# Kernel tuning notes

Measured on AMD Instinct MI355X. Metric: run time of the kernel, lower is better.

## Reference

```python
import jax, jax.numpy as jnp
import numpy as np

EMB = 1024
HEAD = 64


def setup_inputs() -> dict:
    key = jax.random.key(0)
    kx, kq, kk, kv = jax.random.split(key, 4)
    x = jax.random.normal(kx, (4, 4096, EMB), dtype=jnp.float32)
    # nn.Linear(emb, head, bias=False): y = x @ W^T; store transposed [emb, head]
    s = 1.0 / np.sqrt(EMB)
    Wq = jax.random.uniform(kq, (EMB, HEAD), jnp.float32, -s, s)
    Wk = jax.random.uniform(kk, (EMB, HEAD), jnp.float32, -s, s)
    Wv = jax.random.uniform(kv, (EMB, HEAD), jnp.float32, -s, s)
    return {"x": x, "Wq": Wq, "Wk": Wk, "Wv": Wv}


def reference(x, Wq, Wk, Wv):
    # x: [B, T, E]; projections -> [B, T, H]
    Q = jnp.einsum("bte,eh->bth", x, Wq)
    K = jnp.einsum("bte,eh->bth", x, Wk)
    V = jnp.einsum("bte,eh->bth", x, Wv)
    scale = 1.0 / np.sqrt(HEAD).astype(np.float32)
    scores = jnp.einsum("bqh,bkh->bqk", Q, K) * scale  # [B, T, T]
    attn = jax.nn.softmax(scores, axis=-1)
    out = jnp.einsum("bqk,bkh->bqh", attn, V)  # [B, T, H]
    return out
```

## Files before the change

kernel.cpp:

```cpp
#include <hip/hip_runtime.h>
#include <hip/hip_bf16.h>

typedef __bf16 bf16x8 __attribute__((ext_vector_type(8)));
typedef float floatx4 __attribute__((ext_vector_type(4)));

#define B_ 4
#define T_ 4096
#define E_ 1024
#define H_ 64
#define NSEG 8
#define SEGLEN (T_ / NSEG)
#define NROWS (B_ * T_)

#define QSCALE 0.18033688011112042f

#if __has_builtin(__builtin_amdgcn_exp2f)
#define EXP2(x) __builtin_amdgcn_exp2f(x)
#else
#define EXP2(x) exp2f(x)
#endif

__device__ __forceinline__ floatx4 mfma16(bf16x8 a, bf16x8 b, floatx4 c) {
  return __builtin_amdgcn_mfma_f32_16x16x32_bf16(a, b, c, 0, 0, 0);
}

#define GLDS16(gp, lp)                                                        \
  __builtin_amdgcn_global_load_lds(                                           \
      (const __attribute__((address_space(1))) void*)(gp),                    \
      (__attribute__((address_space(3))) void*)(lp), 16, 0, 0)

#define WAITCNT_VM(n) asm volatile("s_waitcnt vmcnt(" #n ")" ::: "memory")
#define WAITCNT_LGKM0 asm volatile("s_waitcnt lgkmcnt(0)" ::: "memory")

__global__ void prep_wt_k(const float* __restrict__ Wq, const float* __restrict__ Wk,
                          const float* __restrict__ Wv, __bf16* __restrict__ Wfrag) {
  int gid = blockIdx.x * 4 + (threadIdx.x >> 6);
  int lane = threadIdx.x & 63;
  int ch = gid / 24, rem = gid % 24;
  int nt = rem >> 1, half = rem & 1;
  int g = lane >> 4, lm = lane & 15;
  int w = nt >> 2;
  const float* W = (w == 0) ? Wq : (w == 1) ? Wk : Wv;
  float sc = (w == 0) ? QSCALE : 1.0f;
  int h = (nt & 3) * 16 + lm;
  int e0 = ch * 64 + half * 32 + g * 8;
  __bf16* dst = Wfrag + (size_t)gid * 1024 / 2 + lane * 8;
  bf16x8 v;
#pragma unroll
  for (int j = 0; j < 8; j++) v[j] = (__bf16)(W[(size_t)(e0 + j) * H_ + h] * sc);
  *(bf16x8*)dst = v;
}

__global__ __launch_bounds__(256) void proj_k(
    const float* __restrict__ x, const __bf16* __restrict__ Wfrag,
    __bf16* __restrict__ Qo, __bf16* __restrict__ Ko, __bf16* __restrict__ Vt) {
  __shared__ __align__(16) char sW[2 * 24576];
  __shared__ __align__(16) char sX[2 * 4096];

  int tid = threadIdx.x;
  int wv = tid >> 6, lane = tid & 63;
  int lm = lane & 15, g = lane >> 4;
  int row_base = blockIdx.x * 32;

  const char* wfb = (const char*)Wfrag;

  int xrow = tid >> 3, xc = tid & 7;
  const float* xsrc = x + (size_t)(row_base + xrow) * E_ + xc * 8;
  int xw_off = xrow * 128 + ((xc ^ (xrow & 7)) << 4);

  int aoff[2][2];
#pragma unroll
  for (int rg = 0; rg < 2; rg++)
#pragma unroll
    for (int ks = 0; ks < 2; ks++)
      aoff[rg][ks] = (rg * 16 + lm) * 128 + ((((ks << 2) + g) ^ (lm & 7)) << 4);

#define STAGE_W(buf, ch)                                                      \
  _Pragma("unroll") for (int j = 0; j < 6; j++)                               \
      GLDS16(wfb + (size_t)(ch) * 24576 + j * 4096 + tid * 16,                \
             sW + (buf) * 24576 + j * 4096 + tid * 16);

#define CVT_X(fA, fB, xv)                                                     \
  {                                                                           \
    xv[0] = (__bf16)fA.x; xv[1] = (__bf16)fA.y;                               \
    xv[2] = (__bf16)fA.z; xv[3] = (__bf16)fA.w;                               \
    xv[4] = (__bf16)fB.x; xv[5] = (__bf16)fB.y;                               \
    xv[6] = (__bf16)fB.z; xv[7] = (__bf16)fB.w;                               \
  }

  floatx4 acc[2][3];
#pragma unroll
  for (int rg = 0; rg < 2; rg++)
#pragma unroll
    for (int i = 0; i < 3; i++) acc[rg][i] = (floatx4)0.0f;

  float4 fA = *(const float4*)(xsrc);
  float4 fB = *(const float4*)(xsrc + 4);
  STAGE_W(0, 0);
  WAITCNT_VM(6);
  __builtin_amdgcn_sched_barrier(0);
  {
    bf16x8 xv; CVT_X(fA, fB, xv);
    *(bf16x8*)(sX + xw_off) = xv;
  }
  WAITCNT_LGKM0;

  for (int ch = 0; ch < 16; ch++) {
    if (ch < 15) {
      fA = *(const float4*)(xsrc + (ch + 1) * 64);
      fB = *(const float4*)(xsrc + (ch + 1) * 64 + 4);
      STAGE_W((ch + 1) & 1, ch + 1);
      WAITCNT_VM(8);
    } else {
      WAITCNT_VM(0);
    }
    __builtin_amdgcn_sched_barrier(0);
    __builtin_amdgcn_s_barrier();

    const char* wB = sW + (ch & 1) * 24576 + (size_t)(wv * 3 * 2) * 1024 + lane * 16;
    const char* xB = sX + (ch & 1) * 4096;
    bf16x8 a[2][2];
#pragma unroll
    for (int rg = 0; rg < 2; rg++)
#pragma unroll
      for (int ks = 0; ks < 2; ks++)
        a[rg][ks] = *(const bf16x8*)(xB + aoff[rg][ks]);
#pragma unroll
    for (int i = 0; i < 3; i++) {
      bf16x8 b0 = *(const bf16x8*)(wB + (size_t)(i * 2) * 1024);
      bf16x8 b1 = *(const bf16x8*)(wB + (size_t)(i * 2 + 1) * 1024);
#pragma unroll
      for (int rg = 0; rg < 2; rg++) {
        acc[rg][i] = mfma16(a[rg][0], b0, acc[rg][i]);
        acc[rg][i] = mfma16(a[rg][1], b1, acc[rg][i]);
      }
    }

    if (ch < 15) {
      WAITCNT_VM(6);
      __builtin_amdgcn_sched_barrier(0);
      bf16x8 xv; CVT_X(fA, fB, xv);
      *(bf16x8*)(sX + ((ch + 1) & 1) * 4096 + xw_off) = xv;
      WAITCNT_LGKM0;
      __builtin_amdgcn_s_barrier();
    }
  }

#pragma unroll
  for (int i = 0; i < 3; i++) {
    int nt = wv * 3 + i;
    int w = nt >> 2;
    int h = (nt & 3) * 16 + lm;
#pragma unroll
    for (int rg = 0; rg < 2; rg++)
#pragma unroll
      for (int r = 0; r < 4; r++) {
        __bf16 v = (__bf16)acc[rg][i][r];
        int rr = row_base + rg * 16 + g * 4 + r;
        if (w == 0)      Qo[(size_t)rr * H_ + h] = v;
        else if (w == 1) Ko[(size_t)rr * H_ + h] = v;
        else {
          int b = rr >> 12, t = rr & (T_ - 1);
          int kin = t & 63;
          int pos = ((kin >> 5) << 5) + (((kin >> 2) & 3) << 3) +
                    (((kin >> 4) & 1) << 2) + (kin & 3);
          Vt[((size_t)b * H_ + h) * T_ + (t & ~63) + pos] = v;
        }
      }
  }
}

__global__ __launch_bounds__(256, 2) void attn_k(
    const __bf16* __restrict__ Q, const __bf16* __restrict__ K,
    const __bf16* __restrict__ Vt, __bf16* __restrict__ Op, float* __restrict__ lp) {
  __shared__ __align__(16) char sK[2 * 8192];
  __shared__ __align__(16) char sV[2 * 8192];

  int qb = blockIdx.x, b = blockIdx.y, seg = blockIdx.z;
  int tid = threadIdx.x, wv = tid >> 6, lane = tid & 63;
  int lm = lane & 15, g = lane >> 4;
  int q0 = qb * 256 + wv * 64;

  const __bf16* Qb = Q + (size_t)b * T_ * H_;
  const char* Kb = (const char*)(K + (size_t)b * T_ * H_);
  const char* Vb = (const char*)(Vt + (size_t)b * H_ * T_);

  bf16x8 qf[4][2];
#pragma unroll
  for (int qi = 0; qi < 4; qi++)
#pragma unroll
    for (int hs = 0; hs < 2; hs++)
      qf[qi][hs] =
          *(const bf16x8*)&Qb[(size_t)(q0 + qi * 16 + lm) * H_ + hs * 32 + g * 8];

  floatx4 o_acc[4][4], o_l[4];
#pragma unroll
  for (int qi = 0; qi < 4; qi++) {
#pragma unroll
    for (int i = 0; i < 4; i++) o_acc[qi][i] = (floatx4)0.0f;
    o_l[qi] = (floatx4)0.0f;
  }

  bf16x8 vone;
#pragma unroll
  for (int j = 0; j < 8; j++) vone[j] = (__bf16)1.0f;

  int s3 = lm & 7;
  int koff[4][2], voff[2][4];
#pragma unroll
  for (int mt = 0; mt < 4; mt++) {
    koff[mt][0] = (mt * 16 + lm) * 128 + ((g ^ s3) << 4);
    koff[mt][1] = (mt * 16 + lm) * 128 + (((g + 4) ^ s3) << 4);
  }
#pragma unroll
  for (int ks = 0; ks < 2; ks++)
#pragma unroll
    for (int nt = 0; nt < 4; nt++)
      voff[ks][nt] = (nt * 16 + lm) * 128 + (((ks * 4 + g) ^ s3) << 4);

  int srow = tid >> 3, schk = tid & 7;
  int swz0 = (schk ^ (srow & 7)) << 4;

#define ATTN_STAGE(buf, k0_)                                                  \
  {                                                                           \
    int off = (buf) * 8192 + tid * 16;                                        \
    GLDS16(Kb + (size_t)(k0_ + srow) * 128 + swz0, sK + off);                 \
    GLDS16(Kb + (size_t)(k0_ + srow + 32) * 128 + swz0, sK + off + 4096);     \
    GLDS16(Vb + (size_t)srow * (T_ * 2) + (size_t)(k0_) * 2 + swz0, sV + off);\
    GLDS16(Vb + (size_t)(srow + 32) * (T_ * 2) + (size_t)(k0_) * 2 + swz0,    \
           sV + off + 4096);                                                  \
  }

  int kbase = seg * SEGLEN;
  ATTN_STAGE(0, kbase);
  __syncthreads();

  for (int t = 0; t < SEGLEN / 64; t++) {
    if (t + 1 < SEGLEN / 64) ATTN_STAGE((t + 1) & 1, kbase + (t + 1) * 64);
    const char* kB = sK + (t & 1) * 8192;
    const char* vB = sV + (t & 1) * 8192;

    floatx4 s_acc[4][4];
#pragma unroll
    for (int mt = 0; mt < 4; mt++)
#pragma unroll
      for (int qi = 0; qi < 4; qi++) s_acc[mt][qi] = (floatx4)0.0f;
#pragma unroll
    for (int mt = 0; mt < 4; mt++) {
      bf16x8 a0 = *(const bf16x8*)(kB + koff[mt][0]);
      bf16x8 a1 = *(const bf16x8*)(kB + koff[mt][1]);
#pragma unroll
      for (int qi = 0; qi < 4; qi++) {
        s_acc[mt][qi] = mfma16(a0, qf[qi][0], s_acc[mt][qi]);
        s_acc[mt][qi] = mfma16(a1, qf[qi][1], s_acc[mt][qi]);
      }
    }

    bf16x8 pa[4][2];
#pragma unroll
    for (int qi = 0; qi < 4; qi++)
#pragma unroll
      for (int mt = 0; mt < 4; mt++)
#pragma unroll
        for (int r = 0; r < 4; r++)
          pa[qi][mt >> 1][(mt & 1) * 4 + r] = (__bf16)EXP2(s_acc[mt][qi][r]);

#pragma unroll
    for (int ks = 0; ks < 2; ks++) {
      bf16x8 bb[4];
#pragma unroll
      for (int nt = 0; nt < 4; nt++) bb[nt] = *(const bf16x8*)(vB + voff[ks][nt]);
#pragma unroll
      for (int qi = 0; qi < 4; qi++) {
#pragma unroll
        for (int nt = 0; nt < 4; nt++)
          o_acc[qi][nt] = mfma16(pa[qi][ks], bb[nt], o_acc[qi][nt]);
        o_l[qi] = mfma16(pa[qi][ks], vone, o_l[qi]);
      }
    }
    __syncthreads();
  }

  size_t rowbase = (size_t)seg * NROWS + (size_t)b * T_ + qb * 256 + wv * 64;
#pragma unroll
  for (int qi = 0; qi < 4; qi++) {
#pragma unroll
    for (int nt = 0; nt < 4; nt++)
#pragma unroll
      for (int r = 0; r < 4; r++)
        Op[(rowbase + qi * 16 + g * 4 + r) * 64 + nt * 16 + lm] =
            (__bf16)o_acc[qi][nt][r];
    if (lm == 0) {
#pragma unroll
      for (int r = 0; r < 4; r++)
        lp[rowbase + qi * 16 + g * 4 + r] = o_l[qi][r];
    }
  }
}

__global__ void combine_k(const __bf16* __restrict__ Op, const float* __restrict__ lp,
                          float* __restrict__ out) {
  int base = (blockIdx.x * 256 + threadIdx.x) * 8;
  int row = base >> 6;
  float L = 0.0f;
  float o[8];
#pragma unroll
  for (int j = 0; j < 8; j++) o[j] = 0.0f;
#pragma unroll
  for (int s = 0; s < NSEG; s++) {
    L += lp[(size_t)s * NROWS + row];
    bf16x8 v = *(const bf16x8*)&Op[(size_t)s * NROWS * 64 + base];
#pragma unroll
    for (int j = 0; j < 8; j++) o[j] += (float)v[j];
  }
  float inv = 1.0f / L;
  float4 r0 = {o[0] * inv, o[1] * inv, o[2] * inv, o[3] * inv};
  float4 r1 = {o[4] * inv, o[5] * inv, o[6] * inv, o[7] * inv};
  *(float4*)&out[base] = r0;
  *(float4*)&out[base + 4] = r1;
}

extern "C" void kernel_launch(void* const* d_in, const int* in_sizes, int n_in,
                              void* d_out, int out_size, void* d_ws, size_t ws_size,
                              hipStream_t stream) {
  const float* x  = (const float*)d_in[0];
  const float* Wq = (const float*)d_in[1];
  const float* Wk = (const float*)d_in[2];
  const float* Wv = (const float*)d_in[3];
  float* out = (float*)d_out;

  char* ws = (char*)d_ws;
  __bf16* Wf  = (__bf16*)(ws);
  __bf16* Qs  = (__bf16*)(ws + 0x60000);
  __bf16* Ks  = (__bf16*)(ws + 0x260000);
  __bf16* Vts = (__bf16*)(ws + 0x460000);
  __bf16* Op  = (__bf16*)(ws + 0x660000);
  float*  lp  = (float*)(ws + 0x1660000);

  prep_wt_k<<<96, 256, 0, stream>>>(Wq, Wk, Wv, Wf);
  proj_k<<<NROWS / 32, 256, 0, stream>>>(x, Wf, Qs, Ks, Vts);
  attn_k<<<dim3(T_ / 256, B_, NSEG), 256, 0, stream>>>(Qs, Ks, Vts, Op, lp);
  combine_k<<<NROWS * 64 / (256 * 8), 256, 0, stream>>>(Op, lp, out);
}
```

Before: 56.34 us.

## Stage fp32 x via direct-to-LDS loads and keep weight fragments in registers

```diff
diff --git a/kernel.cpp b/kernel.cpp
--- a/kernel.cpp
+++ b/kernel.cpp
@@ -30,7 +30,6 @@
       (__attribute__((address_space(3))) void*)(lp), 16, 0, 0)
 
 #define WAITCNT_VM(n) asm volatile("s_waitcnt vmcnt(" #n ")" ::: "memory")
-#define WAITCNT_LGKM0 asm volatile("s_waitcnt lgkmcnt(0)" ::: "memory")
 
 __global__ void prep_wt_k(const float* __restrict__ Wq, const float* __restrict__ Wk,
                           const float* __restrict__ Wv, __bf16* __restrict__ Wfrag) {
@@ -51,84 +50,82 @@
   *(bf16x8*)dst = v;
 }
 
-__global__ __launch_bounds__(256) void proj_k(
+__global__ __launch_bounds__(256, 2) void proj_k(
     const float* __restrict__ x, const __bf16* __restrict__ Wfrag,
     __bf16* __restrict__ Qo, __bf16* __restrict__ Ko, __bf16* __restrict__ Vt) {
-  __shared__ __align__(16) char sW[2 * 24576];
-  __shared__ __align__(16) char sX[2 * 4096];
+  __shared__ __align__(16) char sX[4 * 8192];
 
   int tid = threadIdx.x;
   int wv = tid >> 6, lane = tid & 63;
   int lm = lane & 15, g = lane >> 4;
   int row_base = blockIdx.x * 32;
 
-  const char* wfb = (const char*)Wfrag;
-
-  int xrow = tid >> 3, xc = tid & 7;
-  const float* xsrc = x + (size_t)(row_base + xrow) * E_ + xc * 8;
-  int xw_off = xrow * 128 + ((xc ^ (xrow & 7)) << 4);
-
-  int aoff[2][2];
+  const char* xb = (const char*)x;
+  const char* wfb = (const char*)Wfrag + (size_t)(wv * 3 * 2) * 1024 + lane * 16;
+
+  int xrow[2], xswz[2];
+#pragma unroll
+  for (int i = 0; i < 2; i++) {
+    int s = i * 256 + tid;
+    xrow[i] = s >> 4;
+    xswz[i] = ((s & 15) ^ (xrow[i] & 15)) << 4;
+  }
+
+#define STAGE_X(buf, ch)                                                      \
+  _Pragma("unroll") for (int i = 0; i < 2; i++)                               \
+      GLDS16(xb + (size_t)(row_base + xrow[i]) * 4096 + (size_t)(ch) * 256 +  \
+                 xswz[i],                                                     \
+             sX + (buf) * 8192 + (i * 256 + tid) * 16);
+
+  bf16x8 wreg[2][6];
+#define LOAD_W(set, ch)                                                       \
+  _Pragma("unroll") for (int j = 0; j < 6; j++)                               \
+      wreg[set][j] = *(const bf16x8*)(wfb + ((size_t)(ch) * 24 + j) * 1024);
+
+  floatx4 acc[2][3];
 #pragma unroll
   for (int rg = 0; rg < 2; rg++)
 #pragma unroll
-    for (int ks = 0; ks < 2; ks++)
-      aoff[rg][ks] = (rg * 16 + lm) * 128 + ((((ks << 2) + g) ^ (lm & 7)) << 4);
-
-#define STAGE_W(buf, ch)                                                      \
-  _Pragma("unroll") for (int j = 0; j < 6; j++)                               \
-      GLDS16(wfb + (size_t)(ch) * 24576 + j * 4096 + tid * 16,                \
-             sW + (buf) * 24576 + j * 4096 + tid * 16);
-
-#define CVT_X(fA, fB, xv)                                                     \
-  {                                                                           \
-    xv[0] = (__bf16)fA.x; xv[1] = (__bf16)fA.y;                               \
-    xv[2] = (__bf16)fA.z; xv[3] = (__bf16)fA.w;                               \
-    xv[4] = (__bf16)fB.x; xv[5] = (__bf16)fB.y;                               \
-    xv[6] = (__bf16)fB.z; xv[7] = (__bf16)fB.w;                               \
-  }
-
-  floatx4 acc[2][3];
-#pragma unroll
-  for (int rg = 0; rg < 2; rg++)
-#pragma unroll
     for (int i = 0; i < 3; i++) acc[rg][i] = (floatx4)0.0f;
 
-  float4 fA = *(const float4*)(xsrc);
-  float4 fB = *(const float4*)(xsrc + 4);
-  STAGE_W(0, 0);
-  WAITCNT_VM(6);
+  STAGE_X(0, 0);
+  LOAD_W(0, 0);
   __builtin_amdgcn_sched_barrier(0);
-  {
-    bf16x8 xv; CVT_X(fA, fB, xv);
-    *(bf16x8*)(sX + xw_off) = xv;
-  }
-  WAITCNT_LGKM0;
-
+  STAGE_X(1, 1);
+  LOAD_W(1, 1);
+
+#pragma unroll
   for (int ch = 0; ch < 16; ch++) {
     if (ch < 15) {
-      fA = *(const float4*)(xsrc + (ch + 1) * 64);
-      fB = *(const float4*)(xsrc + (ch + 1) * 64 + 4);
-      STAGE_W((ch + 1) & 1, ch + 1);
       WAITCNT_VM(8);
     } else {
       WAITCNT_VM(0);
     }
     __builtin_amdgcn_sched_barrier(0);
     __builtin_amdgcn_s_barrier();
-
-    const char* wB = sW + (ch & 1) * 24576 + (size_t)(wv * 3 * 2) * 1024 + lane * 16;
-    const char* xB = sX + (ch & 1) * 4096;
+    __builtin_amdgcn_sched_barrier(0);
+
+    if (ch < 14) STAGE_X((ch + 2) & 3, ch + 2);
+
+    const char* xB = sX + (ch & 3) * 8192;
     bf16x8 a[2][2];
 #pragma unroll
     for (int rg = 0; rg < 2; rg++)
 #pragma unroll
-      for (int ks = 0; ks < 2; ks++)
-        a[rg][ks] = *(const bf16x8*)(xB + aoff[rg][ks]);
+      for (int ks = 0; ks < 2; ks++) {
+        int c0 = ks * 8 + g * 2;
+        const char* xp = xB + (rg * 16 + lm) * 256;
+        float4 f0 = *(const float4*)(xp + ((c0 ^ lm) << 4));
+        float4 f1 = *(const float4*)(xp + (((c0 + 1) ^ lm) << 4));
+        a[rg][ks][0] = (__bf16)f0.x; a[rg][ks][1] = (__bf16)f0.y;
+        a[rg][ks][2] = (__bf16)f0.z; a[rg][ks][3] = (__bf16)f0.w;
+        a[rg][ks][4] = (__bf16)f1.x; a[rg][ks][5] = (__bf16)f1.y;
+        a[rg][ks][6] = (__bf16)f1.z; a[rg][ks][7] = (__bf16)f1.w;
+      }
 #pragma unroll
     for (int i = 0; i < 3; i++) {
-      bf16x8 b0 = *(const bf16x8*)(wB + (size_t)(i * 2) * 1024);
-      bf16x8 b1 = *(const bf16x8*)(wB + (size_t)(i * 2 + 1) * 1024);
+      bf16x8 b0 = wreg[ch & 1][i * 2];
+      bf16x8 b1 = wreg[ch & 1][i * 2 + 1];
 #pragma unroll
       for (int rg = 0; rg < 2; rg++) {
         acc[rg][i] = mfma16(a[rg][0], b0, acc[rg][i]);
@@ -136,14 +133,7 @@
       }
     }
 
-    if (ch < 15) {
-      WAITCNT_VM(6);
-      __builtin_amdgcn_sched_barrier(0);
-      bf16x8 xv; CVT_X(fA, fB, xv);
-      *(bf16x8*)(sX + ((ch + 1) & 1) * 4096 + xw_off) = xv;
-      WAITCNT_LGKM0;
-      __builtin_amdgcn_s_barrier();
-    }
+    if (ch < 14) LOAD_W(ch & 1, ch + 2);
   }
 
 #pragma unroll
```

Result: faster. 53.41 us (-5.2%).
